# Kernel tuning notes

Measured on AMD Instinct MI355X. Metric: run time of the kernel, lower is better.

The kernel has to match this reference:

```python
import jax, jax.numpy as jnp
import numpy as np
from jax import lax

TWN_THRESHOLD_FACTOR = 0.05


def ternary_quantize(w, t):
    # codes in {-1, 0, +1}
    return (w > t).astype(w.dtype) - (w < -t).astype(w.dtype)


def setup_inputs() -> dict:
    key = jax.random.key(0)
    kx, kw, kb = jax.random.split(key, 3)
    x = jax.random.normal(kx, (32, 128, 56, 56), dtype=jnp.float32)
    weight = jax.random.normal(kw, (256, 128, 3, 3), dtype=jnp.float32)
    bias = jax.random.normal(kb, (256,), dtype=jnp.float32)
    return {"x": x, "weight": weight, "bias": bias}


def reference(x, weight, bias):
    # threshold from detached weights (matches weight.detach().abs().max())
    threshold = TWN_THRESHOLD_FACTOR * jnp.max(jnp.abs(lax.stop_gradient(weight)))
    q_weight = ternary_quantize(weight, threshold)
    out = lax.conv_general_dilated(
        x, q_weight,
        window_strides=(1, 1),
        padding="VALID",  # F.conv2d default padding=0
        dimension_numbers=("NCHW", "OIHW", "NCHW"),
    )
    return out + bias[None, :, None, None]
```

## Files before the change

kernel.cpp:

```cpp
#include <hip/hip_runtime.h>
#include <hip/hip_bf16.h>
#include <stdint.h>

#define NB   32
#define CIN  128
#define HIN  56
#define WIN  56
#define KOUT 256
#define HOUT 54
#define WOUT 54
#define PQ   (HOUT*WOUT)
#define NPIX (NB*PQ)
#define KK   (CIN*9)
#define HW   (HIN*WIN)
#define TWN_FACTOR 0.05f

typedef short bf16x8 __attribute__((ext_vector_type(8)));
typedef float f32x4  __attribute__((ext_vector_type(4)));

__device__ __forceinline__ void glds16(const void* g, void* l) {
  __builtin_amdgcn_global_load_lds(
      (__attribute__((address_space(1))) void*)(g),
      (__attribute__((address_space(3))) void*)(l),
      16, 0, 0);
}

__global__ void prep_k(const float* __restrict__ x, const float4* __restrict__ w4,
                       float* __restrict__ amax, __hip_bfloat16* __restrict__ xt) {
  __shared__ __hip_bfloat16 tl[64 * 130 + 32];
  __shared__ float sm[4];
  int bid = blockIdx.x;
  int t   = threadIdx.x;

  if (bid < 288) {
    float4 v = w4[bid * 256 + t];
    float m = fmaxf(fmaxf(fabsf(v.x), fabsf(v.y)), fmaxf(fabsf(v.z), fabsf(v.w)));
    #pragma unroll
    for (int off = 32; off > 0; off >>= 1)
      m = fmaxf(m, __shfl_down(m, off));
    int lane = t & 63, wv = t >> 6;
    if (lane == 0) sm[wv] = m;
    __syncthreads();
    if (t == 0)
      atomicMax(amax, fmaxf(fmaxf(sm[0], sm[1]), fmaxf(sm[2], sm[3])));
    return;
  }

  int b2 = bid - 288;
  int n  = b2 / 49, pc = b2 - n * 49;
  const float* xb = x + (size_t)n * CIN * HW + pc * 64;
  int f4 = t & 15, c0 = t >> 4;
  #pragma unroll
  for (int rd = 0; rd < 8; ++rd) {
    int c = c0 + rd * 16;
    float4 v = *(const float4*)(xb + (size_t)c * HW + f4 * 4);
    tl[(f4 * 4 + 0) * 130 + c] = __float2bfloat16(v.x);
    tl[(f4 * 4 + 1) * 130 + c] = __float2bfloat16(v.y);
    tl[(f4 * 4 + 2) * 130 + c] = __float2bfloat16(v.z);
    tl[(f4 * 4 + 3) * 130 + c] = __float2bfloat16(v.w);
  }
  __syncthreads();
  int cc = t & 15, p0 = t >> 4;
  __hip_bfloat16* op = xt + ((size_t)n * HW + pc * 64) * CIN + cc * 8;
  #pragma unroll
  for (int p = p0; p < 64; p += 16)
    *(bf16x8*)(op + (size_t)p * CIN) = *(const bf16x8*)&tl[p * 130 + cc * 8];
}

__global__ void quant_k(const float* __restrict__ w, const float* __restrict__ amax,
                        __hip_bfloat16* __restrict__ qA) {
  float thr = TWN_FACTOR * (*amax);
  int t  = blockIdx.x * 256 + threadIdx.x;
  int kc = t >> 8, row = t & 255;
  int rs = kc >> 4, c0 = (kc & 15) << 3;
  bf16x8 q;
  #pragma unroll
  for (int j = 0; j < 8; ++j) {
    float v  = w[(size_t)(row * CIN + c0 + j) * 9 + rs];
    float qq = (v > thr) ? 1.f : ((v < -thr) ? -1.f : 0.f);
    q[j] = (short)__bfloat16_as_ushort(__float2bfloat16(qq));
  }
  *(bf16x8*)(qA + (size_t)t * 8) = q;
}

__global__ __launch_bounds__(256) void conv_gemm(
    const __hip_bfloat16* __restrict__ xt,
    const __hip_bfloat16* __restrict__ qA,
    const float* __restrict__ bias,
    float* __restrict__ out) {
  __shared__ __hip_bfloat16 Bs[128 * 128];

  const int tid  = threadIdx.x;
  const int wave = tid >> 6;
  const int lane = tid & 63;
  const int quad = lane >> 4;
  const int l16  = lane & 15;

  const int bid   = blockIdx.x;
  const int ktile = bid & 1;
  const int ptile = bid >> 1;
  const int k0    = ktile * 128;
  const int pbase = ptile * 128;

  const int drow = lane >> 4;
  const int pos  = lane & 15;
  unsigned boff[8];
  #pragma unroll
  for (int m = 0; m < 8; ++m) {
    int row  = wave * 32 + m * 4 + drow;
    int prow = pbase + row;
    int n = prow / PQ; int rm = prow - n * PQ;
    int p = rm / WOUT; int q = rm - p * WOUT;
    boff[m] = (unsigned)(n * HW + p * WIN + q) * CIN + ((pos ^ (row & 15)) << 3);
  }
  char* BsB  = (char*)Bs;
  char* bdst = BsB + wave * 8192;

  const int wm = (wave >> 1) * 64;
  const int wn = (wave & 1) * 64;

  unsigned aoff[4];
  #pragma unroll
  for (int i = 0; i < 4; ++i)
    aoff[i] = (unsigned)(quad * 256 + (k0 + wm + i * 16 + l16)) * 8;

  f32x4 acc[4][4];
  #pragma unroll
  for (int i = 0; i < 4; ++i)
    #pragma unroll
    for (int j = 0; j < 4; ++j)
      acc[i][j] = (f32x4){0.f, 0.f, 0.f, 0.f};

  #pragma unroll
  for (int rs = 0; rs < 9; ++rs) {
    const int r = rs / 3, s = rs - r * 3;
    const unsigned bstep = (unsigned)((r * WIN + s) * CIN);

    __syncthreads();
    #pragma unroll
    for (int m = 0; m < 8; ++m)
      glds16(xt + bstep + boff[m], bdst + m * 1024);
    __syncthreads();

    #pragma unroll
    for (int h = 0; h < 4; ++h) {
      bf16x8 af[4], bfr[4];
      #pragma unroll
      for (int i = 0; i < 4; ++i)
        af[i] = *(const bf16x8*)(qA + aoff[i] + (unsigned)(rs * 16 + h * 4) * 2048);
      #pragma unroll
      for (int i = 0; i < 4; ++i) {
        int row = wn + i * 16 + l16;
        bfr[i] = *(const bf16x8*)(BsB + row * 256 + (((h * 4 + quad) ^ l16) << 4));
      }
      #pragma unroll
      for (int i = 0; i < 4; ++i)
        #pragma unroll
        for (int j = 0; j < 4; ++j)
          acc[i][j] = __builtin_amdgcn_mfma_f32_16x16x32_bf16(af[i], bfr[j], acc[i][j], 0, 0, 0);
    }
  }

  const float4* b4 = (const float4*)bias;
  #pragma unroll
  for (int j = 0; j < 4; ++j) {
    int pix  = pbase + wn + j * 16 + l16;
    int nimg = pix / PQ;
    int pq   = pix - nimg * PQ;
    size_t obase = (size_t)nimg * (KOUT * PQ) + pq;
    #pragma unroll
    for (int i = 0; i < 4; ++i) {
      int kb = k0 + wm + i * 16 + quad * 4;
      float4 bv = b4[kb >> 2];
      out[obase + (size_t)(kb + 0) * PQ] = acc[i][j][0] + bv.x;
      out[obase + (size_t)(kb + 1) * PQ] = acc[i][j][1] + bv.y;
      out[obase + (size_t)(kb + 2) * PQ] = acc[i][j][2] + bv.z;
      out[obase + (size_t)(kb + 3) * PQ] = acc[i][j][3] + bv.w;
    }
  }
}

extern "C" void kernel_launch(void* const* d_in, const int* in_sizes, int n_in,
                              void* d_out, int out_size, void* d_ws, size_t ws_size,
                              hipStream_t stream) {
  const float* x    = (const float*)d_in[0];
  const float* w    = (const float*)d_in[1];
  const float* bias = (const float*)d_in[2];
  float* out = (float*)d_out;

  float* amax = (float*)d_ws;
  __hip_bfloat16* xt = (__hip_bfloat16*)((char*)d_ws + 256);
  __hip_bfloat16* qA = (__hip_bfloat16*)((char*)d_ws + 256 + (size_t)NB * HW * CIN * 2);

  prep_k  <<<dim3(1856), dim3(256), 0, stream>>>(x, (const float4*)w, amax, xt);
  quant_k <<<dim3(144),  dim3(256), 0, stream>>>(w, amax, qA);
  conv_gemm<<<dim3(1458), dim3(256), 0, stream>>>(xt, qA, bias, out);
}
```

Measured before the change: 226.6 us.

## Load conv input fragments directly from global memory instead of LDS staging

The shared-memory tile for the activation operand, its global_load_lds fill and both per-tap barriers are removed. Each wave now reads its B fragments straight from the transposed bf16 input in global memory, using precomputed per-pixel offsets. This drops the LDS traffic and block synchronisation. In exchange, pairs of waves load the same data redundantly, and MFMA issue is exposed to global/L2 latency without any staging or prefetch.

```diff
diff --git a/kernel.cpp b/kernel.cpp
--- a/kernel.cpp
+++ b/kernel.cpp
@@ -17,13 +17,6 @@
 
 typedef short bf16x8 __attribute__((ext_vector_type(8)));
 typedef float f32x4  __attribute__((ext_vector_type(4)));
-
-__device__ __forceinline__ void glds16(const void* g, void* l) {
-  __builtin_amdgcn_global_load_lds(
-      (__attribute__((address_space(1))) void*)(g),
-      (__attribute__((address_space(3))) void*)(l),
-      16, 0, 0);
-}
 
 __global__ void prep_k(const float* __restrict__ x, const float4* __restrict__ w4,
                        float* __restrict__ amax, __hip_bfloat16* __restrict__ xt) {
@@ -88,8 +81,6 @@
     const __hip_bfloat16* __restrict__ qA,
     const float* __restrict__ bias,
     float* __restrict__ out) {
-  __shared__ __hip_bfloat16 Bs[128 * 128];
-
   const int tid  = threadIdx.x;
   const int wave = tid >> 6;
   const int lane = tid & 63;
@@ -102,22 +93,17 @@
   const int k0    = ktile * 128;
   const int pbase = ptile * 128;
 
-  const int drow = lane >> 4;
-  const int pos  = lane & 15;
-  unsigned boff[8];
-  #pragma unroll
-  for (int m = 0; m < 8; ++m) {
-    int row  = wave * 32 + m * 4 + drow;
-    int prow = pbase + row;
-    int n = prow / PQ; int rm = prow - n * PQ;
-    int p = rm / WOUT; int q = rm - p * WOUT;
-    boff[m] = (unsigned)(n * HW + p * WIN + q) * CIN + ((pos ^ (row & 15)) << 3);
-  }
-  char* BsB  = (char*)Bs;
-  char* bdst = BsB + wave * 8192;
-
   const int wm = (wave >> 1) * 64;
   const int wn = (wave & 1) * 64;
+
+  unsigned pb[4];
+  #pragma unroll
+  for (int i = 0; i < 4; ++i) {
+    int pix = pbase + wn + i * 16 + l16;
+    int n = pix / PQ; int rm = pix - n * PQ;
+    int p = rm / WOUT; int q = rm - p * WOUT;
+    pb[i] = (unsigned)(n * HW + p * WIN + q) * CIN + quad * 8;
+  }
 
   unsigned aoff[4];
   #pragma unroll
@@ -135,24 +121,17 @@
   for (int rs = 0; rs < 9; ++rs) {
     const int r = rs / 3, s = rs - r * 3;
     const unsigned bstep = (unsigned)((r * WIN + s) * CIN);
-
-    __syncthreads();
-    #pragma unroll
-    for (int m = 0; m < 8; ++m)
-      glds16(xt + bstep + boff[m], bdst + m * 1024);
-    __syncthreads();
+    const unsigned astep = (unsigned)rs * 16 * 2048;
 
     #pragma unroll
     for (int h = 0; h < 4; ++h) {
       bf16x8 af[4], bfr[4];
       #pragma unroll
       for (int i = 0; i < 4; ++i)
-        af[i] = *(const bf16x8*)(qA + aoff[i] + (unsigned)(rs * 16 + h * 4) * 2048);
+        af[i] = *(const bf16x8*)(qA + aoff[i] + astep + (unsigned)h * 4 * 2048);
       #pragma unroll
-      for (int i = 0; i < 4; ++i) {
-        int row = wn + i * 16 + l16;
-        bfr[i] = *(const bf16x8*)(BsB + row * 256 + (((h * 4 + quad) ^ l16) << 4));
-      }
+      for (int i = 0; i < 4; ++i)
+        bfr[i] = *(const bf16x8*)(xt + pb[i] + bstep + (unsigned)h * 32);
       #pragma unroll
       for (int i = 0; i < 4; ++i)
         #pragma unroll
```

Result: slower. 289.8 us (+27.9%).

## Double-buffer input tile in LDS with half-channel stages to overlap loads

Applied to the files above, without the earlier changes.

The conv GEMM now splits each 3x3 tap's 128-channel B tile into two 64-channel halves held in two LDS buffers. The load for the next stage is issued before computing on the current one, so global-to-LDS traffic overlaps the MFMA work instead of sitting between two barriers. The XOR swizzle is adjusted to 8 chunks per 64-channel row. In exchange there are 18 barriered stages instead of 9. There is also no explicit vmcnt wait before the barrier, so the correctness of the async global_load_lds relies on the barrier ordering.

```diff
diff --git a/kernel.cpp b/kernel.cpp
--- a/kernel.cpp
+++ b/kernel.cpp
@@ -88,7 +88,7 @@
     const __hip_bfloat16* __restrict__ qA,
     const float* __restrict__ bias,
     float* __restrict__ out) {
-  __shared__ __hip_bfloat16 Bs[128 * 128];
+  __shared__ __hip_bfloat16 Bs[2][128 * 64];
 
   const int tid  = threadIdx.x;
   const int wave = tid >> 6;
@@ -102,22 +102,20 @@
   const int k0    = ktile * 128;
   const int pbase = ptile * 128;
 
-  const int drow = lane >> 4;
-  const int pos  = lane & 15;
-  unsigned boff[8];
-  #pragma unroll
-  for (int m = 0; m < 8; ++m) {
-    int row  = wave * 32 + m * 4 + drow;
+  const int wm = (wave >> 1) * 64;
+  const int wn = (wave & 1) * 64;
+
+  const int r8 = lane >> 3;
+  const int ch = lane & 7;
+  unsigned boffm[4];
+  #pragma unroll
+  for (int m = 0; m < 4; ++m) {
+    int row  = wave * 32 + m * 8 + r8;
     int prow = pbase + row;
     int n = prow / PQ; int rm = prow - n * PQ;
     int p = rm / WOUT; int q = rm - p * WOUT;
-    boff[m] = (unsigned)(n * HW + p * WIN + q) * CIN + ((pos ^ (row & 15)) << 3);
-  }
-  char* BsB  = (char*)Bs;
-  char* bdst = BsB + wave * 8192;
-
-  const int wm = (wave >> 1) * 64;
-  const int wn = (wave & 1) * 64;
+    boffm[m] = (unsigned)(n * HW + p * WIN + q) * CIN + ((ch ^ (row & 7)) << 3);
+  }
 
   unsigned aoff[4];
   #pragma unroll
@@ -131,27 +129,40 @@
     for (int j = 0; j < 4; ++j)
       acc[i][j] = (f32x4){0.f, 0.f, 0.f, 0.f};
 
-  #pragma unroll
-  for (int rs = 0; rs < 9; ++rs) {
-    const int r = rs / 3, s = rs - r * 3;
-    const unsigned bstep = (unsigned)((r * WIN + s) * CIN);
-
-    __syncthreads();
-    #pragma unroll
-    for (int m = 0; m < 8; ++m)
-      glds16(xt + bstep + boff[m], bdst + m * 1024);
-    __syncthreads();
-
-    #pragma unroll
-    for (int h = 0; h < 4; ++h) {
+  {
+    char* bdst = (char*)Bs[0] + wave * 4096;
+    #pragma unroll
+    for (int m = 0; m < 4; ++m)
+      glds16(xt + boffm[m], bdst + m * 1024);
+  }
+  __syncthreads();
+
+  #pragma unroll
+  for (int t = 0; t < 18; ++t) {
+    if (t < 17) {
+      const int tn  = t + 1;
+      const int rsn = tn >> 1;
+      const int rn  = rsn / 3, sn = rsn - rn * 3;
+      const unsigned bst = (unsigned)((rn * WIN + sn) * CIN + (tn & 1) * 64);
+      char* bdst = (char*)Bs[tn & 1] + wave * 4096;
+      #pragma unroll
+      for (int m = 0; m < 4; ++m)
+        glds16(xt + boffm[m] + bst, bdst + m * 1024);
+    }
+
+    const char* bp = (const char*)Bs[t & 1];
+    const unsigned astep = ((unsigned)(t >> 1) * 16 + (unsigned)(t & 1) * 8) * 2048;
+
+    #pragma unroll
+    for (int h = 0; h < 2; ++h) {
       bf16x8 af[4], bfr[4];
       #pragma unroll
       for (int i = 0; i < 4; ++i)
-        af[i] = *(const bf16x8*)(qA + aoff[i] + (unsigned)(rs * 16 + h * 4) * 2048);
+        af[i] = *(const bf16x8*)(qA + aoff[i] + astep + (unsigned)h * 4 * 2048);
       #pragma unroll
       for (int i = 0; i < 4; ++i) {
         int row = wn + i * 16 + l16;
-        bfr[i] = *(const bf16x8*)(BsB + row * 256 + (((h * 4 + quad) ^ l16) << 4));
+        bfr[i] = *(const bf16x8*)(bp + (row * 64 + (((h * 4 + quad) ^ (row & 7)) << 3)) * 2);
       }
       #pragma unroll
       for (int i = 0; i < 4; ++i)
@@ -159,6 +170,7 @@
         for (int j = 0; j < 4; ++j)
           acc[i][j] = __builtin_amdgcn_mfma_f32_16x16x32_bf16(af[i], bfr[j], acc[i][j], 0, 0, 0);
     }
+    __syncthreads();
   }
 
   const float4* b4 = (const float4*)bias;
```

Result: faster. 218.6 us (-3.5%).
